# Performance work log

Hardware: AMD Instinct MI355X
Metric: run time of the kernel (lower is better)

## Reference

```python
import jax, jax.numpy as jnp
import numpy as np

B, S, HID = 2, 2048, 4096
NH, NKV, HD = 32, 8, 128
MAX_POS = 4096
SCALE = HD ** -0.5


def _rope_tables():
    inv_freq = 1.0 / (10000.0 ** (np.arange(0, HD, 2, dtype=np.float32) / HD))
    t = np.arange(MAX_POS, dtype=np.float32)
    freqs = np.outer(t, inv_freq)              # [MAX_POS, HD/2]
    emb = np.concatenate([freqs, freqs], axis=-1)  # [MAX_POS, HD]
    return jnp.asarray(np.cos(emb)), jnp.asarray(np.sin(emb))


def setup_inputs() -> dict:
    key = jax.random.key(0)
    ks = jax.random.split(key, 6)
    hidden_states = jax.random.normal(ks[0], (B, S, HID), dtype=jnp.float32)
    position_ids = jnp.broadcast_to(jnp.arange(S, dtype=jnp.int64 if jax.config.jax_enable_x64 else jnp.int32), (B, S))
    cos_table, sin_table = _rope_tables()
    # weights stored [in, out] for x @ W
    sd = HID ** -0.5
    Wq = jax.random.normal(ks[1], (HID, NH * HD), dtype=jnp.float32) * sd
    Wk = jax.random.normal(ks[2], (HID, NKV * HD), dtype=jnp.float32) * sd
    Wv = jax.random.normal(ks[3], (HID, NKV * HD), dtype=jnp.float32) * sd
    Wo = jax.random.normal(ks[4], (NH * HD, HID), dtype=jnp.float32) * sd
    return {"hidden_states": hidden_states, "position_ids": position_ids,
            "cos_table": cos_table, "sin_table": sin_table,
            "Wq": Wq, "Wk": Wk, "Wv": Wv, "Wo": Wo}


def _rotate_half(x):
    x1, x2 = jnp.split(x, 2, axis=-1)
    return jnp.concatenate([-x2, x1], axis=-1)


def reference(hidden_states, position_ids, cos_table, sin_table, Wq, Wk, Wv, Wo):
    b, s, _ = hidden_states.shape
    q = (hidden_states @ Wq).reshape(b, s, NH, HD)
    k = (hidden_states @ Wk).reshape(b, s, NKV, HD)
    v = (hidden_states @ Wv).reshape(b, s, NKV, HD)

    # RoPE, cos/sin gathered by position and unsqueezed at head dim (dim=2, bsnd)
    cos = cos_table[position_ids][:, :, None, :]  # [b, s, 1, hd]
    sin = sin_table[position_ids][:, :, None, :]
    q = q * cos + _rotate_half(q) * sin
    k = k * cos + _rotate_half(k) * sin

    # GQA: expand kv heads to match query heads
    rep = NH // NKV
    k = jnp.repeat(k, rep, axis=2)  # [b, s, NH, hd]
    v = jnp.repeat(v, rep, axis=2)

    scores = jnp.einsum('bqnd,bknd->bnqk', q, k) * SCALE  # [b, NH, s, s]
    causal = jnp.tril(jnp.ones((s, s), dtype=bool))
    scores = jnp.where(causal, scores, jnp.finfo(scores.dtype).min)
    probs = jax.nn.softmax(scores, axis=-1)
    attn = jnp.einsum('bnqk,bknd->bqnd', probs, v)  # [b, s, NH, hd]
    attn = attn.reshape(b, s, NH * HD)
    return attn @ Wo
```

## Files before the change

### kernel.cpp

```cpp
#include <hip/hip_runtime.h>
#include <stdint.h>

typedef unsigned short u16;
typedef __bf16 bf16x8 __attribute__((ext_vector_type(8)));
typedef unsigned short u16x8 __attribute__((ext_vector_type(8)));
typedef unsigned short u16x4 __attribute__((ext_vector_type(4)));
typedef float f32x4 __attribute__((ext_vector_type(4)));

#define B_ 2
#define S_ 2048
#define HID_ 4096
#define NH_ 32
#define NKV_ 8
#define HD_ 128
#define NTOT_ 6144
#define SCALE_ 0.08838834764831845f

#define GLD16(gp, lp)                                                     \
  __builtin_amdgcn_global_load_lds(                                       \
      (__attribute__((address_space(1))) void*)(gp),                      \
      (__attribute__((address_space(3))) void*)(lp), 16, 0, 0)

#define BAR __builtin_amdgcn_s_barrier()
#define PRIO1 __builtin_amdgcn_s_setprio(1)
#define PRIO0 __builtin_amdgcn_s_setprio(0)
#define VM8 asm volatile("s_waitcnt vmcnt(8)" ::: "memory")
#define VM0 asm volatile("s_waitcnt vmcnt(0)" ::: "memory")

__device__ __forceinline__ u16 f2b(float f) {
  union { float f; uint32_t u; } v; v.f = f;
  uint32_t u = v.u;
  u = u + 0x7fffu + ((u >> 16) & 1u);
  return (u16)(u >> 16);
}
__device__ __forceinline__ float b2f(u16 s) {
  union { uint32_t u; float f; } v; v.u = ((uint32_t)s) << 16;
  return v.f;
}
__device__ __forceinline__ bf16x8 ldb8(const u16* p) {
  u16x8 u = *(const u16x8*)p;
  return __builtin_bit_cast(bf16x8, u);
}
__device__ __forceinline__ bf16x8 ldb8b(const char* p) {
  u16x8 u = *(const u16x8*)p;
  return __builtin_bit_cast(bf16x8, u);
}

__global__ __launch_bounds__(256) void k_prep(const float* __restrict__ hs,
                                              u16* __restrict__ Xb,
                                              const float* __restrict__ Wq,
                                              const float* __restrict__ Wk,
                                              const float* __restrict__ Wv,
                                              u16* __restrict__ WqkvT,
                                              const float* __restrict__ Wo,
                                              u16* __restrict__ WoT) {
  __shared__ u16 tile[64][65];
  int bid = blockIdx.x;
  int t = threadIdx.x;
  if (bid < 16384) {
    int i = bid * 256 + t;
    const float4 v = ((const float4*)hs)[i];
    u16x4 o = { f2b(v.x), f2b(v.y), f2b(v.z), f2b(v.w) };
    *(u16x4*)(Xb + (size_t)i * 4) = o;
    return;
  }
  const float* src;
  u16* dst;
  int N, ns, ng, k0;
  const int Kd = HID_;
  if (bid < 16384 + 6144) {
    int ti = bid - 16384;
    k0 = (ti & 63) * 64;
    ng = (ti >> 6) * 64;
    dst = WqkvT;
    if (ng < 4096)      { src = Wq; N = 4096; ns = ng; }
    else if (ng < 5120) { src = Wk; N = 1024; ns = ng - 4096; }
    else                { src = Wv; N = 1024; ns = ng - 5120; }
  } else {
    int ti = bid - 16384 - 6144;
    k0 = (ti & 63) * 64;
    ng = (ti >> 6) * 64;
    src = Wo; dst = WoT; N = 4096; ns = ng;
  }
  int rr = t >> 4;
  int cc = (t & 15) * 4;
#pragma unroll
  for (int p = 0; p < 4; ++p) {
    int r = p * 16 + rr;
    float4 v = *(const float4*)&src[(size_t)(k0 + r) * N + ns + cc];
    tile[cc + 0][r] = f2b(v.x);
    tile[cc + 1][r] = f2b(v.y);
    tile[cc + 2][r] = f2b(v.z);
    tile[cc + 3][r] = f2b(v.w);
  }
  __syncthreads();
#pragma unroll
  for (int p = 0; p < 4; ++p) {
    int n = p * 16 + rr;
    u16x4 o = { tile[n][cc], tile[n][cc + 1], tile[n][cc + 2], tile[n][cc + 3] };
    *(u16x4*)&dst[(size_t)(ng + n) * Kd + k0 + cc] = o;
  }
}

__global__ __launch_bounds__(512) void k_gemm_out(const u16* __restrict__ A,
                                                  const u16* __restrict__ Bt,
                                                  float* __restrict__ Cf,
                                                  int M, int N, int Kd) {
  __shared__ __align__(16) char smem[131072];
  const int NT = Kd >> 6;

  int nwg = gridDim.x * gridDim.y;
  int orig = blockIdx.y * gridDim.x + blockIdx.x;
  int cpx = nwg >> 3;
  int swz = (orig & 7) * cpx + (orig >> 3);
  int bx = swz % gridDim.x, by = swz / gridDim.x;
  int m0 = by * 256, n0 = bx * 256;

  int t = threadIdx.x, lane = t & 63, wave = t >> 6;
  int wr = wave >> 2, wc = wave & 3;
  int lg = lane >> 4, l16 = lane & 15;
  int loff = l16 * 64 + ((lg ^ ((l16 >> 1) & 3)) << 4);
  int srow = lane >> 2, schk = (lane & 3) ^ ((lane >> 3) & 3);

  const u16* Asrc = A  + (size_t)(m0 + wave * 32 + srow) * Kd + schk * 8;
  const u16* Bsrc = Bt + (size_t)(n0 + wave * 32 + srow) * Kd + schk * 8;

  f32x4 acc[8][4] = {};

#define OST_A(tile, kc, BB) do {                                              \
    char* d_ = smem + (BB) + ((kc) << 14) + (wave << 11);                     \
    const u16* s_ = Asrc + (size_t)(tile) * 64 + (kc) * 32;                   \
    GLD16(s_, d_); GLD16(s_ + (size_t)16 * Kd, d_ + 1024); } while (0)
#define OST_B(tile, kc, BB) do {                                              \
    char* d_ = smem + (BB) + 32768 + ((kc) << 14) + (wave << 11);             \
    const u16* s_ = Bsrc + (size_t)(tile) * 64 + (kc) * 32;                   \
    GLD16(s_, d_); GLD16(s_ + (size_t)16 * Kd, d_ + 1024); } while (0)
#define OLDB(BB, kc) do { _Pragma("unroll")                                   \
    for (int j = 0; j < 4; ++j)                                               \
      bfr[j] = ldb8b(smem + (BB) + 32768 + ((kc) << 14) + ((wc * 4 + j) << 10) + loff); } while (0)
#define OLDA(BB, kc, mh) do { _Pragma("unroll")                               \
    for (int i = 0; i < 4; ++i)                                               \
      af[i] = ldb8b(smem + (BB) + ((kc) << 14) + ((wr * 8 + (mh) * 4 + i) << 10) + loff); } while (0)
#define OMFMA(mh) do { _Pragma("unroll")                                      \
    for (int i = 0; i < 4; ++i) { _Pragma("unroll")                           \
      for (int j = 0; j < 4; ++j)                                             \
        acc[(mh) * 4 + i][j] = __builtin_amdgcn_mfma_f32_16x16x32_bf16(af[i], bfr[j], acc[(mh) * 4 + i][j], 0, 0, 0); } } while (0)

  OST_A(0, 0, 0); OST_B(0, 0, 0); OST_A(0, 1, 0); OST_B(0, 1, 0);
  OST_A(1, 0, 65536); OST_B(1, 0, 65536);
  VM8; BAR;

  for (int it = 0; it < (NT >> 1); ++it) {
    int a = it << 1;
    bool pf = (a + 2 < NT);
    bf16x8 bfr[4], af[4];
    OLDB(0, 0); OLDA(0, 0, 0); OST_A(a + 1, 1, 65536);
    PRIO1; OMFMA(0); PRIO0;
    OLDA(0, 0, 1); OST_B(a + 1, 1, 65536);
    PRIO1; OMFMA(1); PRIO0; if (pf) { VM8; } else { VM0; } BAR;
    OLDB(0, 1); OLDA(0, 1, 0); if (pf) OST_A(a + 2, 0, 0);
    PRIO1; OMFMA(0); PRIO0;
    OLDA(0, 1, 1); if (pf) OST_B(a + 2, 0, 0);
    PRIO1; OMFMA(1); PRIO0; if (pf) { VM8; } else { VM0; } BAR;
    OLDB(65536, 0); OLDA(65536, 0, 0); if (pf) OST_A(a + 2, 1, 0);
    PRIO1; OMFMA(0); PRIO0;
    OLDA(65536, 0, 1); if (pf) OST_B(a + 2, 1, 0);
    PRIO1; OMFMA(1); PRIO0; if (pf) { VM8; } else { VM0; } BAR;
    OLDB(65536, 1); OLDA(65536, 1, 0); if (pf) OST_A(a + 3, 0, 65536);
    PRIO1; OMFMA(0); PRIO0;
    OLDA(65536, 1, 1); if (pf) OST_B(a + 3, 0, 65536);
    PRIO1; OMFMA(1); PRIO0; if (pf) { VM8; } BAR;
  }
#undef OST_A
#undef OST_B
#undef OLDB
#undef OLDA
#undef OMFMA

#pragma unroll
  for (int i = 0; i < 8; ++i)
#pragma unroll
    for (int j = 0; j < 4; ++j)
#pragma unroll
      for (int r = 0; r < 4; ++r) {
        int m = m0 + wr * 128 + i * 16 + lg * 4 + r;
        int n = n0 + wc * 64 + j * 16 + l16;
        Cf[(size_t)m * N + n] = acc[i][j][r];
      }
}

__global__ __launch_bounds__(512) void k_gqkv(const u16* __restrict__ A,
                                              const u16* __restrict__ Bt,
                                              u16* __restrict__ Qb,
                                              u16* __restrict__ Kb,
                                              u16* __restrict__ Vb) {
  __shared__ __align__(16) char smem[114688];
  const int Kd = HID_;
  const int NT = Kd >> 6;

  int orig = blockIdx.y * 32 + blockIdx.x;
  int swz = (orig & 7) * 64 + (orig >> 3);
  int bx = swz & 31, by = swz >> 5;
  int m0 = by * 256, n0 = bx * 192;

  int t = threadIdx.x, lane = t & 63, wave = t >> 6;
  int wr = wave >> 2, wc = wave & 3;
  int lg = lane >> 4, l16 = lane & 15;
  int loff = l16 * 64 + ((lg ^ ((l16 >> 1) & 3)) << 4);
  int srow = lane >> 2, schk = (lane & 3) ^ ((lane >> 3) & 3);

  const u16* Asrc = A + (size_t)(m0 + wave * 32 + srow) * Kd + schk * 8;
  const u16* sB0 = Bt + (size_t)(n0 + wave * 16 + srow) * Kd + schk * 8;
  const u16* sB1 = Bt + (size_t)(n0 + 128 + (wave & 3) * 16 + srow) * Kd + schk * 8;
  int bdst2 = (8 + (wave & 3)) << 10;

  f32x4 acc[8][3] = {};

#define QST_A(tile, kc, BB) do {                                              \
    char* d_ = smem + (BB) + ((kc) << 14) + (wave << 11);                     \
    const u16* s_ = Asrc + (size_t)(tile) * 64 + (kc) * 32;                   \
    GLD16(s_, d_); GLD16(s_ + (size_t)16 * Kd, d_ + 1024); } while (0)
#define QST_B(tile, kc, BB) do {                                              \
    char* db_ = smem + (BB) + 32768 + (kc) * 12288;                           \
    GLD16(sB0 + (size_t)(tile) * 64 + (kc) * 32, db_ + (wave << 10));         \
    GLD16(sB1 + (size_t)(tile) * 64 + (kc) * 32, db_ + bdst2); } while (0)
#define QLDB(BB, kc) do { _Pragma("unroll")                                   \
    for (int j = 0; j < 3; ++j)                                               \
      bfr[j] = ldb8b(smem + (BB) + 32768 + (kc) * 12288 + ((wc * 3 + j) << 10) + loff); } while (0)
#define QLDA(BB, kc, mh) do { _Pragma("unroll")                               \
    for (int i = 0; i < 4; ++i)                                               \
      af[i] = ldb8b(smem + (BB) + ((kc) << 14) + ((wr * 8 + (mh) * 4 + i) << 10) + loff); } while (0)
#define QMFMA(mh) do { _Pragma("unroll")                                      \
    for (int i = 0; i < 4; ++i) { _Pragma("unroll")                           \
      for (int j = 0; j < 3; ++j)                                             \
        acc[(mh) * 4 + i][j] = __builtin_amdgcn_mfma_f32_16x16x32_bf16(af[i], bfr[j], acc[(mh) * 4 + i][j], 0, 0, 0); } } while (0)

  QST_A(0, 0, 0); QST_B(0, 0, 0); QST_A(0, 1, 0); QST_B(0, 1, 0);
  QST_A(1, 0, 57344); QST_B(1, 0, 57344);
  VM8; BAR;

  for (int it = 0; it < (NT >> 1); ++it) {
    int a = it << 1;
    bool pf = (a + 2 < NT);
    bf16x8 bfr[3], af[4];
    QLDB(0, 0); QLDA(0, 0, 0); QST_A(a + 1, 1, 57344);
    PRIO1; QMFMA(0); PRIO0;
    QLDA(0, 0, 1); QST_B(a + 1, 1, 57344);
    PRIO1; QMFMA(1); PRIO0; if (pf) { VM8; } else { VM0; } BAR;
    QLDB(0, 1); QLDA(0, 1, 0); if (pf) QST_A(a + 2, 0, 0);
    PRIO1; QMFMA(0); PRIO0;
    QLDA(0, 1, 1); if (pf) QST_B(a + 2, 0, 0);
    PRIO1; QMFMA(1); PRIO0; if (pf) { VM8; } else { VM0; } BAR;
    QLDB(57344, 0); QLDA(57344, 0, 0); if (pf) QST_A(a + 2, 1, 0);
    PRIO1; QMFMA(0); PRIO0;
    QLDA(57344, 0, 1); if (pf) QST_B(a + 2, 1, 0);
    PRIO1; QMFMA(1); PRIO0; if (pf) { VM8; } else { VM0; } BAR;
    QLDB(57344, 1); QLDA(57344, 1, 0); if (pf) QST_A(a + 3, 0, 57344);
    PRIO1; QMFMA(0); PRIO0;
    QLDA(57344, 1, 1); if (pf) QST_B(a + 3, 0, 57344);
    PRIO1; QMFMA(1); PRIO0; if (pf) { VM8; } BAR;
  }
#undef QST_A
#undef QST_B
#undef QLDB
#undef QLDA
#undef QMFMA

#pragma unroll
  for (int i = 0; i < 8; ++i)
#pragma unroll
    for (int j = 0; j < 3; ++j)
#pragma unroll
      for (int r = 0; r < 4; ++r) {
        int m = m0 + wr * 128 + i * 16 + lg * 4 + r;
        int n = n0 + wc * 48 + j * 16 + l16;
        int head = n >> 7, d = n & 127;
        int b = m >> 11, s = m & (S_ - 1);
        u16 val = f2b(acc[i][j][r]);
        if (head < NH_) {
          Qb[(((size_t)b * NH_ + head) * S_ + s) * HD_ + d] = val;
        } else if (head < NH_ + NKV_) {
          Kb[(((size_t)b * NKV_ + (head - NH_)) * S_ + s) * HD_ + d] = val;
        } else {
          Vb[(((size_t)b * NKV_ + (head - NH_ - NKV_)) * HD_ + d) * S_ + s] = val;
        }
      }
}

__global__ __launch_bounds__(256) void k_ropek(u16* __restrict__ Kb,
                                               const int* __restrict__ pos,
                                               const float* __restrict__ ct,
                                               const float* __restrict__ st) {
  int wave = threadIdx.x >> 6, lane = threadIdx.x & 63;
  int row = blockIdx.x * 4 + wave;
  int s = row & (S_ - 1);
  int b = row / (NKV_ * S_);
  int p = pos[b * S_ + s];
  size_t base = (size_t)row * HD_;
  float x1 = b2f(Kb[base + lane]);
  float x2 = b2f(Kb[base + 64 + lane]);
  float c  = ct[(size_t)p * HD_ + lane];
  float sn = st[(size_t)p * HD_ + lane];
  Kb[base + lane]      = f2b(x1 * c - x2 * sn);
  Kb[base + 64 + lane] = f2b(x2 * c + x1 * sn);
}

__global__ __launch_bounds__(256, 4) void k_attn(const u16* __restrict__ Q,
                                                 const u16* __restrict__ K,
                                                 const u16* __restrict__ Vt,
                                                 u16* __restrict__ Ob,
                                                 const int* __restrict__ pos,
                                                 const float* __restrict__ ct,
                                                 const float* __restrict__ st) {
  __shared__ __align__(16) char smem[40960];
  const int VS_OFF = 16384, PS_OFF = 32768;

  int bid = blockIdx.x;
  int pid = bid & 15;
  int h   = (bid >> 4) & 31;
  int b   = bid >> 9;
  int kvh = h >> 2;
  int tid = threadIdx.x;
  int wave = tid >> 6, lane = tid & 63;
  int lg = lane >> 4, l16 = lane & 15;
  int lsw = (l16 & 7) << 4;

  const u16* Qp = Q  + (((size_t)b * NH_  + h)   * S_) * HD_;
  const u16* Kp = K  + (((size_t)b * NKV_ + kvh) * S_) * HD_;
  const u16* Vp = Vt + (((size_t)b * NKV_ + kvh) * HD_) * S_;

  for (int pass = 0; pass < 2; ++pass) {
    int qt = pass ? (31 - pid) : pid;
    int q0 = qt * 64 + wave * 16;
    int qg = q0 + l16;

    u16x8 qu[4];
#pragma unroll
    for (int c = 0; c < 4; ++c)
      qu[c] = *(const u16x8*)&Qp[(size_t)qg * HD_ + c * 32 + lg * 8];
    int prot = pos[b * S_ + qg];
    const float* cb = ct + (size_t)prot * HD_;
    const float* sb = st + (size_t)prot * HD_;
    bf16x8 qf[4];
#pragma unroll
    for (int c = 0; c < 4; ++c) {
      int d0 = c * 32 + lg * 8;
      u16x8 o;
#pragma unroll
      for (int e = 0; e < 8; ++e) {
        float x  = b2f(qu[c][e]);
        float xp = b2f(qu[c ^ 2][e]);
        float cc = cb[d0 + e];
        float ss = sb[d0 + e];
        float res = (c < 2) ? (x * cc - xp * ss) : fmaf(xp, ss, x * cc);
        o[e] = f2b(res);
      }
      qf[c] = __builtin_bit_cast(bf16x8, o);
    }

    f32x4 oacc[8] = {};
    float mrun = -1e30f, lrun = 0.f;

    int nt = qt + 1;
    for (int tI = 0; tI < nt; ++tI) {
      int kb = tI * 64;
      __syncthreads();
#pragma unroll
      for (int i = 0; i < 4; ++i) {
        int ci = i * 256 + tid;
        int r = ci >> 4, ch = ci & 15;
        u16x8 v = *(const u16x8*)&Kp[(size_t)(kb + r) * HD_ + ch * 8];
        *(u16x8*)(smem + r * 256 + ((ch * 16) ^ ((r & 7) << 4))) = v;
      }
#pragma unroll
      for (int i = 0; i < 4; ++i) {
        int ci = i * 256 + tid;
        int r = ci >> 3, ch = ci & 7;
        u16x8 v = *(const u16x8*)&Vp[(size_t)r * S_ + kb + ch * 8];
        *(u16x8*)(smem + VS_OFF + r * 128 + ((ch * 16) ^ ((r & 7) << 4))) = v;
      }
      __syncthreads();

      f32x4 sc[4] = {};
#pragma unroll
      for (int c = 0; c < 4; ++c) {
#pragma unroll
        for (int n = 0; n < 4; ++n) {
          bf16x8 kf = ldb8b(smem + (n * 16 + l16) * 256 + ((c * 64 + lg * 16) ^ lsw));
          sc[n] = __builtin_amdgcn_mfma_f32_16x16x32_bf16(kf, qf[c], sc[n], 0, 0, 0);
        }
      }

      bool diag = (tI == qt);
      float mx = -1e30f;
#pragma unroll
      for (int n = 0; n < 4; ++n)
#pragma unroll
        for (int r = 0; r < 4; ++r) {
          float v = sc[n][r];
          int key = kb + n * 16 + lg * 4 + r;
          if (diag && key > qg) v = -1e30f;
          sc[n][r] = v;
          mx = fmaxf(mx, v);
        }
      mx = fmaxf(mx, __shfl_xor(mx, 16));
      mx = fmaxf(mx, __shfl_xor(mx, 32));
      float mnew = fmaxf(mrun, mx * SCALE_);
      float alpha = __expf(mrun - mnew);
      float ps = 0.f;
#pragma unroll
      for (int n = 0; n < 4; ++n) {
        u16x4 pk;
#pragma unroll
        for (int r = 0; r < 4; ++r) {
          float p = __expf(fmaf(sc[n][r], SCALE_, -mnew));
          ps += p;
          pk[r] = f2b(p);
        }
        *(u16x4*)(smem + PS_OFF + wave * 2048 + l16 * 128 + ((n * 32 + lg * 8) ^ lsw)) = pk;
      }
      ps += __shfl_xor(ps, 16);
      ps += __shfl_xor(ps, 32);
      lrun = lrun * alpha + ps;
      mrun = mnew;

      float ar[4];
#pragma unroll
      for (int r = 0; r < 4; ++r) ar[r] = __shfl(alpha, lg * 4 + r);
#pragma unroll
      for (int ns = 0; ns < 8; ++ns)
#pragma unroll
        for (int r = 0; r < 4; ++r) oacc[ns][r] *= ar[r];

#pragma unroll
      for (int ck = 0; ck < 2; ++ck) {
        bf16x8 pa = ldb8b(smem + PS_OFF + wave * 2048 + l16 * 128 + ((ck * 64 + lg * 16) ^ lsw));
#pragma unroll
        for (int ns = 0; ns < 8; ++ns) {
          bf16x8 vf = ldb8b(smem + VS_OFF + (ns * 16 + l16) * 128 + ((ck * 64 + lg * 16) ^ lsw));
          oacc[ns] = __builtin_amdgcn_mfma_f32_16x16x32_bf16(pa, vf, oacc[ns], 0, 0, 0);
        }
      }
    }

    float lr[4];
#pragma unroll
    for (int r = 0; r < 4; ++r) lr[r] = 1.0f / __shfl(lrun, lg * 4 + r);
#pragma unroll
    for (int ns = 0; ns < 8; ++ns)
#pragma unroll
      for (int r = 0; r < 4; ++r) {
        int q = q0 + lg * 4 + r;
        Ob[((size_t)(b * S_) + q) * (NH_ * HD_) + h * HD_ + ns * 16 + l16] =
            f2b(oacc[ns][r] * lr[r]);
      }
  }
}

extern "C" void kernel_launch(void* const* d_in, const int* in_sizes, int n_in,
                              void* d_out, int out_size, void* d_ws, size_t ws_size,
                              hipStream_t stream) {
  const float* hs  = (const float*)d_in[0];
  const int*   pos = (const int*)d_in[1];
  const float* ct  = (const float*)d_in[2];
  const float* st  = (const float*)d_in[3];
  const float* Wq  = (const float*)d_in[4];
  const float* Wk  = (const float*)d_in[5];
  const float* Wv  = (const float*)d_in[6];
  const float* Wo  = (const float*)d_in[7];
  float* out = (float*)d_out;

  char* w = (char*)d_ws;
  u16* Xb    = (u16*)(w);
  u16* WqkvT = (u16*)(w + 33554432ull);
  u16* WoT   = (u16*)(w + 83886080ull);
  u16* Qb    = (u16*)(w + 117440512ull);
  u16* Kb    = (u16*)(w + 150994944ull);
  u16* Vb    = (u16*)(w + 159383552ull);
  u16* Attb  = (u16*)(w + 167772160ull);

  k_prep<<<26624, 256, 0, stream>>>(hs, Xb, Wq, Wk, Wv, WqkvT, Wo, WoT);
  k_gqkv<<<dim3(32, 16), 512, 0, stream>>>(Xb, WqkvT, Qb, Kb, Vb);
  k_ropek<<<8192, 256, 0, stream>>>(Kb, pos, ct, st);
  k_attn<<<1024, 256, 0, stream>>>(Qb, Kb, Vb, Attb, pos, ct, st);
  k_gemm_out<<<dim3(16, 16), 512, 0, stream>>>(Attb, WoT, out, 4096, 4096, 4096);
}
```

Measured before the change: 591.2 us.

## Retile output GEMM to 128x256 with 3-stage K=32 LDS pipeline

The output projection GEMM moves from 256x256 tiles with a double-buffered K=64 schedule to 128x256 tiles with a triple-buffered K=32 ring. The grid doubles to 512 workgroups, which helps fill the 256 CUs better than the previous 256 tiles did. Shared memory drops from 128KB to 72KB, which may allow more residency. In exchange, each tile reuses data less, there is a barrier every K=32 step, and each wave has fewer MFMAs between waits.

After: 613.6 us. 3.8% more time.

```diff
diff --git a/kernel.cpp b/kernel.cpp
--- a/kernel.cpp
+++ b/kernel.cpp
@@ -25,6 +25,7 @@
 #define PRIO1 __builtin_amdgcn_s_setprio(1)
 #define PRIO0 __builtin_amdgcn_s_setprio(0)
 #define VM8 asm volatile("s_waitcnt vmcnt(8)" ::: "memory")
+#define VM3 asm volatile("s_waitcnt vmcnt(3)" ::: "memory")
 #define VM0 asm volatile("s_waitcnt vmcnt(0)" ::: "memory")
 
 __device__ __forceinline__ u16 f2b(float f) {
@@ -106,15 +107,13 @@
                                                   const u16* __restrict__ Bt,
                                                   float* __restrict__ Cf,
                                                   int M, int N, int Kd) {
-  __shared__ __align__(16) char smem[131072];
-  const int NT = Kd >> 6;
-
-  int nwg = gridDim.x * gridDim.y;
-  int orig = blockIdx.y * gridDim.x + blockIdx.x;
-  int cpx = nwg >> 3;
-  int swz = (orig & 7) * cpx + (orig >> 3);
-  int bx = swz % gridDim.x, by = swz / gridDim.x;
-  int m0 = by * 256, n0 = bx * 256;
+  __shared__ __align__(16) char smem[73728];
+  const int NT = Kd >> 5;
+
+  int orig = blockIdx.y * 16 + blockIdx.x;
+  int swz = (orig & 7) * 64 + (orig >> 3);
+  int bx = swz & 15, by = swz >> 4;
+  int m0 = by * 128, n0 = bx * 256;
 
   int t = threadIdx.x, lane = t & 63, wave = t >> 6;
   int wr = wave >> 2, wc = wave & 3;
@@ -122,68 +121,55 @@
   int loff = l16 * 64 + ((lg ^ ((l16 >> 1) & 3)) << 4);
   int srow = lane >> 2, schk = (lane & 3) ^ ((lane >> 3) & 3);
 
-  const u16* Asrc = A  + (size_t)(m0 + wave * 32 + srow) * Kd + schk * 8;
-  const u16* Bsrc = Bt + (size_t)(n0 + wave * 32 + srow) * Kd + schk * 8;
-
-  f32x4 acc[8][4] = {};
-
-#define OST_A(tile, kc, BB) do {                                              \
-    char* d_ = smem + (BB) + ((kc) << 14) + (wave << 11);                     \
-    const u16* s_ = Asrc + (size_t)(tile) * 64 + (kc) * 32;                   \
-    GLD16(s_, d_); GLD16(s_ + (size_t)16 * Kd, d_ + 1024); } while (0)
-#define OST_B(tile, kc, BB) do {                                              \
-    char* d_ = smem + (BB) + 32768 + ((kc) << 14) + (wave << 11);             \
-    const u16* s_ = Bsrc + (size_t)(tile) * 64 + (kc) * 32;                   \
-    GLD16(s_, d_); GLD16(s_ + (size_t)16 * Kd, d_ + 1024); } while (0)
-#define OLDB(BB, kc) do { _Pragma("unroll")                                   \
-    for (int j = 0; j < 4; ++j)                                               \
-      bfr[j] = ldb8b(smem + (BB) + 32768 + ((kc) << 14) + ((wc * 4 + j) << 10) + loff); } while (0)
-#define OLDA(BB, kc, mh) do { _Pragma("unroll")                               \
-    for (int i = 0; i < 4; ++i)                                               \
-      af[i] = ldb8b(smem + (BB) + ((kc) << 14) + ((wr * 8 + (mh) * 4 + i) << 10) + loff); } while (0)
-#define OMFMA(mh) do { _Pragma("unroll")                                      \
-    for (int i = 0; i < 4; ++i) { _Pragma("unroll")                           \
-      for (int j = 0; j < 4; ++j)                                             \
-        acc[(mh) * 4 + i][j] = __builtin_amdgcn_mfma_f32_16x16x32_bf16(af[i], bfr[j], acc[(mh) * 4 + i][j], 0, 0, 0); } } while (0)
-
-  OST_A(0, 0, 0); OST_B(0, 0, 0); OST_A(0, 1, 0); OST_B(0, 1, 0);
-  OST_A(1, 0, 65536); OST_B(1, 0, 65536);
-  VM8; BAR;
-
-  for (int it = 0; it < (NT >> 1); ++it) {
-    int a = it << 1;
-    bool pf = (a + 2 < NT);
+  const u16* Asrc = A  + (size_t)(m0 + wave * 16 + srow) * Kd + schk * 8;
+  const u16* Bsrc = Bt + (size_t)(n0 + wave * 16 + srow) * Kd + schk * 8;
+  const u16* Bsrc2 = Bsrc + (size_t)128 * Kd;
+
+  f32x4 acc[4][4] = {};
+
+#define OSTG(kt, buf) do {                                                    \
+    GLD16(Asrc  + (size_t)(kt) * 32, (buf) + (wave << 10));                   \
+    GLD16(Bsrc  + (size_t)(kt) * 32, (buf) + 8192 + (wave << 10));            \
+    GLD16(Bsrc2 + (size_t)(kt) * 32, (buf) + 8192 + ((wave + 8) << 10)); } while (0)
+
+  char* p0 = smem;
+  char* p1 = smem + 24576;
+  char* p2 = smem + 49152;
+
+  OSTG(0, p0);
+  OSTG(1, p1);
+  VM3; BAR;
+
+  for (int kt = 0; kt < NT; ++kt) {
     bf16x8 bfr[4], af[4];
-    OLDB(0, 0); OLDA(0, 0, 0); OST_A(a + 1, 1, 65536);
-    PRIO1; OMFMA(0); PRIO0;
-    OLDA(0, 0, 1); OST_B(a + 1, 1, 65536);
-    PRIO1; OMFMA(1); PRIO0; if (pf) { VM8; } else { VM0; } BAR;
-    OLDB(0, 1); OLDA(0, 1, 0); if (pf) OST_A(a + 2, 0, 0);
-    PRIO1; OMFMA(0); PRIO0;
-    OLDA(0, 1, 1); if (pf) OST_B(a + 2, 0, 0);
-    PRIO1; OMFMA(1); PRIO0; if (pf) { VM8; } else { VM0; } BAR;
-    OLDB(65536, 0); OLDA(65536, 0, 0); if (pf) OST_A(a + 2, 1, 0);
-    PRIO1; OMFMA(0); PRIO0;
-    OLDA(65536, 0, 1); if (pf) OST_B(a + 2, 1, 0);
-    PRIO1; OMFMA(1); PRIO0; if (pf) { VM8; } else { VM0; } BAR;
-    OLDB(65536, 1); OLDA(65536, 1, 0); if (pf) OST_A(a + 3, 0, 65536);
-    PRIO1; OMFMA(0); PRIO0;
-    OLDA(65536, 1, 1); if (pf) OST_B(a + 3, 0, 65536);
-    PRIO1; OMFMA(1); PRIO0; if (pf) { VM8; } BAR;
-  }
-#undef OST_A
-#undef OST_B
-#undef OLDB
-#undef OLDA
-#undef OMFMA
-
-#pragma unroll
-  for (int i = 0; i < 8; ++i)
 #pragma unroll
     for (int j = 0; j < 4; ++j)
+      bfr[j] = ldb8b(p0 + 8192 + ((wc * 4 + j) << 10) + loff);
+#pragma unroll
+    for (int i = 0; i < 4; ++i)
+      af[i] = ldb8b(p0 + ((wr * 4 + i) << 10) + loff);
+    bool pf2 = (kt + 2 < NT);
+    if (pf2) OSTG(kt + 2, p2);
+    PRIO1;
+#pragma unroll
+    for (int i = 0; i < 4; ++i)
+#pragma unroll
+      for (int j = 0; j < 4; ++j)
+        acc[i][j] = __builtin_amdgcn_mfma_f32_16x16x32_bf16(af[i], bfr[j], acc[i][j], 0, 0, 0);
+    PRIO0;
+    if (pf2) { VM3; } else if (kt + 1 < NT) { VM0; }
+    BAR;
+    char* tmp = p0; p0 = p1; p1 = p2; p2 = tmp;
+  }
+#undef OSTG
+
+#pragma unroll
+  for (int i = 0; i < 4; ++i)
+#pragma unroll
+    for (int j = 0; j < 4; ++j)
 #pragma unroll
       for (int r = 0; r < 4; ++r) {
-        int m = m0 + wr * 128 + i * 16 + lg * 4 + r;
+        int m = m0 + wr * 64 + i * 16 + lg * 4 + r;
         int n = n0 + wc * 64 + j * 16 + l16;
         Cf[(size_t)m * N + n] = acc[i][j][r];
       }
@@ -483,5 +469,5 @@
   k_gqkv<<<dim3(32, 16), 512, 0, stream>>>(Xb, WqkvT, Qb, Kb, Vb);
   k_ropek<<<8192, 256, 0, stream>>>(Kb, pos, ct, st);
   k_attn<<<1024, 256, 0, stream>>>(Qb, Kb, Vb, Attb, pos, ct, st);
-  k_gemm_out<<<dim3(16, 16), 512, 0, stream>>>(Attb, WoT, out, 4096, 4096, 4096);
-}
+  k_gemm_out<<<dim3(16, 32), 512, 0, stream>>>(Attb, WoT, out, 4096, 4096, 4096);
+}
```
